# Optimization experiments

Measured on AMD Instinct MI355X. Metric: run time of the kernel, lower is better.

## Reference

```python
import jax, jax.numpy as jnp
import numpy as np

EMBED_DIM = 1024
PROJ_DIM = 64
B, S = 8, 2048


def setup_inputs() -> dict:
    key = jax.random.key(0)
    k1, k2, k3 = jax.random.split(key, 3)
    context = jax.random.normal(k1, (S, B, EMBED_DIM), dtype=jnp.float32)
    prior = jax.random.uniform(k2, (B, S), dtype=jnp.float32)
    # xavier_uniform for (2*proj_dim, embed_dim)
    bound = float(np.sqrt(6.0 / (2 * PROJ_DIM + EMBED_DIM)))
    proj_weight = jax.random.uniform(k3, (2 * PROJ_DIM, EMBED_DIM), dtype=jnp.float32,
                                     minval=-bound, maxval=bound)
    proj_bias = jnp.zeros((2 * PROJ_DIM,), dtype=jnp.float32)
    return {"context": context, "prior": prior,
            "proj_weight": proj_weight, "proj_bias": proj_bias}


def reference(context, prior, proj_weight, proj_bias):
    # context: (S, B, E) -> (B, S, E)
    x = jnp.transpose(context, (1, 0, 2))
    b, s, e = x.shape
    qk = jnp.einsum('bse,pe->bsp', x, proj_weight) + proj_bias  # (B,S,2P)
    query, key = jnp.split(qk, 2, axis=2)
    # neighbor scores, scaled by embed_dim (as in the original)
    fwd = jnp.sum(query[:, :-1] * key[:, 1:], axis=-1) / e   # (B,S-1) score i<->i+1
    bwd = jnp.sum(query[:, 1:] * key[:, :-1], axis=-1) / e   # (B,S-1) score i<->i-1
    ninf = jnp.full((b, 1), -jnp.inf, dtype=x.dtype)
    score = jnp.stack([jnp.concatenate([fwd, ninf], axis=1),
                       jnp.concatenate([ninf, bwd], axis=1)], axis=-1)  # (B,S,2)
    prob = jax.nn.softmax(score, axis=-1)
    # torch .roll(shifts=-1) with no dims flattens the whole tensor: reproduce that
    shift_prob = jnp.roll(prob[:, :, 1].reshape(-1), -1).reshape(b, s)
    prob0 = jnp.sqrt(prob[:, :, 0] * shift_prob + 1e-6)      # (B,S)
    neighbor_attn = prior + (1.0 - prior) * prob0
    log_prob = jnp.log(neighbor_attn)
    # Original places log_prob[:, :-1] on the superdiagonal and hits it with
    # triu matmuls on both sides: C[i,j] = sum_{m=i}^{j-1} log_prob[m] for j>i.
    # Equivalent O(n^2): prefix sums cs[t] = sum_{m<t} log_prob[m].
    cs = jnp.concatenate([jnp.zeros((b, 1), dtype=x.dtype),
                          jnp.cumsum(log_prob[:, :-1], axis=1)], axis=1)  # (B,S)
    D = cs[:, None, :] - cs[:, :, None]            # D[b,i,j] = cs[j]-cs[i]
    i_idx = jnp.arange(s)
    upper = i_idx[None, :] > i_idx[:, None]        # (S,S) j>i
    M = jnp.where(upper[None], D, -D)              # C + C^T (symmetric)
    constituent_attn = jnp.exp(M)
    diag = i_idx[None, :] == i_idx[:, None]
    constituent_attn = jnp.where(diag[None], jnp.zeros((), x.dtype), constituent_attn)
    return constituent_attn, neighbor_attn
```

## Files before the change

### kernel.cpp

```cpp
#include <hip/hip_runtime.h>
#include <cstdint>
#include <cstddef>

#define E_DIM 1024
#define PD 64
#define NP 128
#define B_DIM 8
#define S_DIM 2048
#define M_TOT (B_DIM * S_DIM)

#define KH 512
#define BM 64
#define BK 32
#define NCH (KH / BK)

typedef __attribute__((ext_vector_type(8))) short short8v;
typedef __attribute__((ext_vector_type(4))) float f32x4;

__device__ __forceinline__ void gload16(const float* g, float* l) {
    __builtin_amdgcn_global_load_lds(
        (const __attribute__((address_space(1))) unsigned int*)g,
        (__attribute__((address_space(3))) unsigned int*)(uintptr_t)l,
        16, 0, 0);
}

__device__ __forceinline__ void cvt_hilo(const f32x4 v0, const f32x4 v1,
                                         short8v& h, short8v& l) {
    const unsigned MSK = 0xFFFF0000u;
    unsigned a0 = __float_as_uint(v0.x), a1 = __float_as_uint(v0.y);
    unsigned a2 = __float_as_uint(v0.z), a3 = __float_as_uint(v0.w);
    unsigned a4 = __float_as_uint(v1.x), a5 = __float_as_uint(v1.y);
    unsigned a6 = __float_as_uint(v1.z), a7 = __float_as_uint(v1.w);
    float l0 = v0.x - __uint_as_float(a0 & MSK);
    float l1 = v0.y - __uint_as_float(a1 & MSK);
    float l2 = v0.z - __uint_as_float(a2 & MSK);
    float l3 = v0.w - __uint_as_float(a3 & MSK);
    float l4 = v1.x - __uint_as_float(a4 & MSK);
    float l5 = v1.y - __uint_as_float(a5 & MSK);
    float l6 = v1.z - __uint_as_float(a6 & MSK);
    float l7 = v1.w - __uint_as_float(a7 & MSK);
    union { unsigned u[4]; short8v s; } H, L;
    H.u[0] = (a1 & MSK) | (a0 >> 16);
    H.u[1] = (a3 & MSK) | (a2 >> 16);
    H.u[2] = (a5 & MSK) | (a4 >> 16);
    H.u[3] = (a7 & MSK) | (a6 >> 16);
    L.u[0] = (__float_as_uint(l1) & MSK) | (__float_as_uint(l0) >> 16);
    L.u[1] = (__float_as_uint(l3) & MSK) | (__float_as_uint(l2) >> 16);
    L.u[2] = (__float_as_uint(l5) & MSK) | (__float_as_uint(l4) >> 16);
    L.u[3] = (__float_as_uint(l7) & MSK) | (__float_as_uint(l6) >> 16);
    h = H.s; l = L.s;
}

__global__ __launch_bounds__(256, 2) void gemm_qk(const float* __restrict__ A,
                                                  const float* __restrict__ W,
                                                  float* __restrict__ qk0,
                                                  float* __restrict__ qk1) {
    __shared__ float As[2][BM][BK];
    __shared__ float Ws[2][NP][BK];
    const int tid = threadIdx.x;
    const int kh  = blockIdx.x & 1;
    const int m0  = (blockIdx.x >> 1) * BM;
    const int k0  = kh * KH;
    const int w   = __builtin_amdgcn_readfirstlane(tid >> 6);
    const int ln  = tid & 63;

    const int lr   = ln >> 3;
    const int gsrc = ((ln & 7) ^ lr) << 2;
    const float* aS = A + (size_t)(m0 + w * 16 + lr) * E_DIM + k0 + gsrc;
    const float* wS = W + (size_t)(w * 32 + lr) * E_DIM + k0 + gsrc;

    const int row16 = ln & 15;
    const int kq    = ln >> 4;
    const int wm    = (w >> 1) * 32;
    const int wn    = (w & 1) * 64;
    const int sg0   = (((kq << 1) | 0) ^ (row16 & 7)) << 2;
    const int sg1   = (((kq << 1) | 1) ^ (row16 & 7)) << 2;

    float* qkP = kh ? qk1 : qk0;

    f32x4 acc[2][4];
#pragma unroll
    for (int i = 0; i < 2; ++i)
#pragma unroll
        for (int j = 0; j < 4; ++j) acc[i][j] = (f32x4){0.f, 0.f, 0.f, 0.f};

#define STAGE(BUF, KOFF)                                                       \
    {                                                                          \
        gload16(aS + (KOFF),               &As[BUF][w * 16][0]);               \
        gload16(aS + (KOFF) + 8 * E_DIM,   &As[BUF][w * 16 + 8][0]);           \
        gload16(wS + (KOFF),               &Ws[BUF][w * 32][0]);               \
        gload16(wS + (KOFF) + 8 * E_DIM,   &Ws[BUF][w * 32 + 8][0]);           \
        gload16(wS + (KOFF) + 16 * E_DIM,  &Ws[BUF][w * 32 + 16][0]);          \
        gload16(wS + (KOFF) + 24 * E_DIM,  &Ws[BUF][w * 32 + 24][0]);          \
    }

    STAGE(0, 0)

    for (int ch = 0; ch < NCH; ++ch) {
        const int buf = ch & 1;
        __syncthreads();
        if (ch + 1 < NCH) {
            STAGE(buf ^ 1, (ch + 1) * BK)
        }
        short8v ah[2], al[2], wh[4], wl[4];
#pragma unroll
        for (int fi = 0; fi < 2; ++fi) {
            const float* base = &As[buf][wm + fi * 16 + row16][0];
            const f32x4 v0 = *(const f32x4*)(base + sg0);
            const f32x4 v1 = *(const f32x4*)(base + sg1);
            cvt_hilo(v0, v1, ah[fi], al[fi]);
        }
#pragma unroll
        for (int fj = 0; fj < 4; ++fj) {
            const float* base = &Ws[buf][wn + fj * 16 + row16][0];
            const f32x4 v0 = *(const f32x4*)(base + sg0);
            const f32x4 v1 = *(const f32x4*)(base + sg1);
            cvt_hilo(v0, v1, wh[fj], wl[fj]);
        }
#pragma unroll
        for (int fi = 0; fi < 2; ++fi)
#pragma unroll
            for (int fj = 0; fj < 4; ++fj) {
                acc[fi][fj] = __builtin_amdgcn_mfma_f32_16x16x32_bf16(
                    ah[fi], wh[fj], acc[fi][fj], 0, 0, 0);
                acc[fi][fj] = __builtin_amdgcn_mfma_f32_16x16x32_bf16(
                    ah[fi], wl[fj], acc[fi][fj], 0, 0, 0);
                acc[fi][fj] = __builtin_amdgcn_mfma_f32_16x16x32_bf16(
                    al[fi], wh[fj], acc[fi][fj], 0, 0, 0);
            }
    }
#undef STAGE

#pragma unroll
    for (int fi = 0; fi < 2; ++fi)
#pragma unroll
        for (int fj = 0; fj < 4; ++fj) {
#pragma unroll
            for (int r = 0; r < 4; ++r) {
                const int m = m0 + wm + fi * 16 + kq * 4 + r;
                const int p = wn + fj * 16 + row16;
                qkP[(size_t)m * NP + p] = acc[fi][fj][r];
            }
        }
}

__global__ __launch_bounds__(256) void neighbor_probs(const float* __restrict__ qk0,
                                                      const float* __restrict__ qk1,
                                                      const float* __restrict__ bias,
                                                      float* __restrict__ p0,
                                                      float* __restrict__ p1) {
    const int m = blockIdx.x * 4 + (threadIdx.x >> 6);
    const int lane = threadIdx.x & 63;
    const int s = m >> 3;
    const int b = m & 7;

    const float bq = bias[lane];
    const float bk = bias[PD + lane];
    const size_t oq = (size_t)m * NP + lane;
    const float q = qk0[oq] + qk1[oq] + bq;
    float kn = 0.f, kp = 0.f;
    if (s < S_DIM - 1) {
        const size_t o = (size_t)(m + B_DIM) * NP + PD + lane;
        kn = qk0[o] + qk1[o] + bk;
    }
    if (s > 0) {
        const size_t o = (size_t)(m - B_DIM) * NP + PD + lane;
        kp = qk0[o] + qk1[o] + bk;
    }
    float f = q * kn;
    float g = q * kp;
#pragma unroll
    for (int off = 32; off; off >>= 1) {
        f += __shfl_xor(f, off);
        g += __shfl_xor(g, off);
    }
    if (lane == 0) {
        const float s0 = f * (1.f / (float)E_DIM);
        const float s1 = g * (1.f / (float)E_DIM);
        float P0, P1;
        if (s == S_DIM - 1) { P0 = 0.f; P1 = 1.f; }
        else if (s == 0)    { P0 = 1.f; P1 = 0.f; }
        else {
            const float mx = fmaxf(s0, s1);
            const float e0 = __expf(s0 - mx), e1 = __expf(s1 - mx);
            const float inv = 1.f / (e0 + e1);
            P0 = e0 * inv; P1 = e1 * inv;
        }
        p0[b * S_DIM + s] = P0;
        p1[b * S_DIM + s] = P1;
    }
}

__global__ __launch_bounds__(256) void combine_scan(const float* __restrict__ p0,
                                                    const float* __restrict__ p1,
                                                    const float* __restrict__ prior,
                                                    float* __restrict__ out_na,
                                                    float* __restrict__ cs) {
    const int b = blockIdx.x;
    const int tid = threadIdx.x;
    __shared__ float sh[256];

    const int base = b * S_DIM + tid * 8;
    float incl[8];
    float run = 0.f;
#pragma unroll
    for (int u = 0; u < 8; ++u) {
        const int fidx = base + u;
        int nf = fidx + 1;
        if (nf == B_DIM * S_DIM) nf = 0;
        const float P0 = p0[fidx];
        const float sp = p1[nf];
        const float pr = prior[fidx];
        const float na = pr + (1.f - pr) * sqrtf(P0 * sp + 1e-6f);
        out_na[fidx] = na;
        run += __logf(na);
        incl[u] = run;
    }
    sh[tid] = run;
    __syncthreads();
    for (int off = 1; off < 256; off <<= 1) {
        float v = sh[tid];
        if (tid >= off) v += sh[tid - off];
        __syncthreads();
        sh[tid] = v;
        __syncthreads();
    }
    const float offset = (tid > 0) ? sh[tid - 1] : 0.f;
#pragma unroll
    for (int u = 0; u < 8; ++u) {
        cs[base + u] = offset + ((u > 0) ? incl[u - 1] : 0.f);
    }
}

__global__ __launch_bounds__(256) void big_out(const float* __restrict__ cs,
                                               float* __restrict__ out) {
    const int bi = blockIdx.x;
    const int b = bi >> 11;
    const int i = bi & (S_DIM - 1);
    const float ci = cs[b * S_DIM + i];
    const float* crow = cs + (size_t)b * S_DIM;
    float* orow = out + (size_t)bi * S_DIM;
    const int j0 = threadIdx.x * 8;
#pragma unroll
    for (int h = 0; h < 2; ++h) {
        const int j = j0 + h * 4;
        const float4 cj = *(const float4*)&crow[j];
        float4 o;
        {
            const int jj = j + 0; const float m = (jj > i) ? (cj.x - ci) : (ci - cj.x);
            o.x = (jj == i) ? 0.f : __expf(m);
        }
        {
            const int jj = j + 1; const float m = (jj > i) ? (cj.y - ci) : (ci - cj.y);
            o.y = (jj == i) ? 0.f : __expf(m);
        }
        {
            const int jj = j + 2; const float m = (jj > i) ? (cj.z - ci) : (ci - cj.z);
            o.z = (jj == i) ? 0.f : __expf(m);
        }
        {
            const int jj = j + 3; const float m = (jj > i) ? (cj.w - ci) : (ci - cj.w);
            o.w = (jj == i) ? 0.f : __expf(m);
        }
        *(float4*)&orow[j] = o;
    }
}

extern "C" void kernel_launch(void* const* d_in, const int* in_sizes, int n_in,
                              void* d_out, int out_size, void* d_ws, size_t ws_size,
                              hipStream_t stream) {
    const float* context = (const float*)d_in[0];
    const float* prior   = (const float*)d_in[1];
    const float* W       = (const float*)d_in[2];
    const float* bias    = (const float*)d_in[3];
    float* out = (float*)d_out;

    float* qk0 = (float*)d_ws;
    float* p0  = qk0 + (size_t)M_TOT * NP;
    float* p1  = p0 + M_TOT;
    float* cs  = p1 + M_TOT;
    float* qk1 = out;
    float* na_out = out + (size_t)B_DIM * S_DIM * S_DIM;

    gemm_qk<<<(M_TOT / BM) * 2, 256, 0, stream>>>(context, W, qk0, qk1);
    neighbor_probs<<<M_TOT / 4, 256, 0, stream>>>(qk0, qk1, bias, p0, p1);
    combine_scan<<<B_DIM, 256, 0, stream>>>(p0, p1, prior, na_out, cs);
    big_out<<<M_TOT, 256, 0, stream>>>(cs, out);
}
```

Measured before the change: 66.62 us.

## Pre-split weights into bf16 hi/lo images and drop split-K in QK GEMM

A new kernel converts the projection weight once per call into packed bf16 hi/lo images laid out for direct LDS staging. The GEMM then skips per-tile weight conversion, runs over the full K without split-K, and uses smaller 32-row tiles with each wave owning 32 output columns. Bias is added in the GEMM epilogue, so the neighbor kernel reads one qk buffer instead of summing two partials. The big output kernel also switches to nontemporal stores. The cost is an extra launch and loss of the split-K parallelism, with a longer K loop per block.

New measurement: 84.66 us. 27.1% more time.

```diff
diff --git a/kernel.cpp b/kernel.cpp
--- a/kernel.cpp
+++ b/kernel.cpp
@@ -9,15 +9,14 @@
 #define S_DIM 2048
 #define M_TOT (B_DIM * S_DIM)
 
-#define KH 512
-#define BM 64
+#define BMR 32
 #define BK 32
-#define NCH (KH / BK)
+#define NCH (E_DIM / BK)
 
 typedef __attribute__((ext_vector_type(8))) short short8v;
 typedef __attribute__((ext_vector_type(4))) float f32x4;
 
-__device__ __forceinline__ void gload16(const float* g, float* l) {
+__device__ __forceinline__ void gload16(const void* g, void* l) {
     __builtin_amdgcn_global_load_lds(
         (const __attribute__((address_space(1))) unsigned int*)g,
         (__attribute__((address_space(3))) unsigned int*)(uintptr_t)l,
@@ -51,47 +50,64 @@
     h = H.s; l = L.s;
 }
 
+__global__ __launch_bounds__(256) void conv_w(const float* __restrict__ W,
+                                              ushort* __restrict__ hiImg,
+                                              ushort* __restrict__ loImg) {
+    const int t = blockIdx.x * 256 + threadIdx.x;
+    const int c  = t & 127;
+    const int q  = (t >> 7) & 3;
+    const int ch = t >> 9;
+    const float* src = W + (size_t)c * E_DIM + ch * 32 + q * 8;
+    const f32x4 v0 = *(const f32x4*)src;
+    const f32x4 v1 = *(const f32x4*)(src + 4);
+    short8v h, l;
+    cvt_hilo(v0, v1, h, l);
+    const size_t off = ((size_t)(ch * 4 + q) * NP + c) * 8;
+    *(short8v*)&hiImg[off] = h;
+    *(short8v*)&loImg[off] = l;
+}
+
 __global__ __launch_bounds__(256, 2) void gemm_qk(const float* __restrict__ A,
-                                                  const float* __restrict__ W,
-                                                  float* __restrict__ qk0,
-                                                  float* __restrict__ qk1) {
-    __shared__ float As[2][BM][BK];
-    __shared__ float Ws[2][NP][BK];
+                                                  const ushort* __restrict__ hiImg,
+                                                  const ushort* __restrict__ loImg,
+                                                  const float* __restrict__ bias,
+                                                  float* __restrict__ qk) {
+    __shared__ __align__(16) float  As[2][BMR][BK];
+    __shared__ __align__(16) ushort Whi[2][4][NP][8];
+    __shared__ __align__(16) ushort Wlo[2][4][NP][8];
     const int tid = threadIdx.x;
-    const int kh  = blockIdx.x & 1;
-    const int m0  = (blockIdx.x >> 1) * BM;
-    const int k0  = kh * KH;
+    const int m0  = blockIdx.x * BMR;
     const int w   = __builtin_amdgcn_readfirstlane(tid >> 6);
     const int ln  = tid & 63;
-
-    const int lr   = ln >> 3;
-    const int gsrc = ((ln & 7) ^ lr) << 2;
-    const float* aS = A + (size_t)(m0 + w * 16 + lr) * E_DIM + k0 + gsrc;
-    const float* wS = W + (size_t)(w * 32 + lr) * E_DIM + k0 + gsrc;
-
+    const int lr  = ln >> 3;
+    const int g8  = ln & 7;
     const int row16 = ln & 15;
     const int kq    = ln >> 4;
-    const int wm    = (w >> 1) * 32;
-    const int wn    = (w & 1) * 64;
-    const int sg0   = (((kq << 1) | 0) ^ (row16 & 7)) << 2;
-    const int sg1   = (((kq << 1) | 1) ^ (row16 & 7)) << 2;
-
-    float* qkP = kh ? qk1 : qk0;
-
-    f32x4 acc[2][4];
+    const int r7    = row16 & 7;
+    const int sg0 = ((((kq << 1) | 0) ^ r7) & 7) << 2;
+    const int sg1 = ((((kq << 1) | 1) ^ r7) & 7) << 2;
+
+    const float*  aS = A + (size_t)(m0 + w * 8 + lr) * E_DIM + ((g8 ^ lr) << 2);
+    const ushort* hS = hiImg + (size_t)(w * 2) * 512 + ln * 8;
+    const ushort* lS = loImg + (size_t)(w * 2) * 512 + ln * 8;
+
+    float bias2[2];
+    bias2[0] = bias[w * 32 + row16];
+    bias2[1] = bias[w * 32 + 16 + row16];
+
+    f32x4 acc[2][2];
 #pragma unroll
     for (int i = 0; i < 2; ++i)
 #pragma unroll
-        for (int j = 0; j < 4; ++j) acc[i][j] = (f32x4){0.f, 0.f, 0.f, 0.f};
-
-#define STAGE(BUF, KOFF)                                                       \
-    {                                                                          \
-        gload16(aS + (KOFF),               &As[BUF][w * 16][0]);               \
-        gload16(aS + (KOFF) + 8 * E_DIM,   &As[BUF][w * 16 + 8][0]);           \
-        gload16(wS + (KOFF),               &Ws[BUF][w * 32][0]);               \
-        gload16(wS + (KOFF) + 8 * E_DIM,   &Ws[BUF][w * 32 + 8][0]);           \
-        gload16(wS + (KOFF) + 16 * E_DIM,  &Ws[BUF][w * 32 + 16][0]);          \
-        gload16(wS + (KOFF) + 24 * E_DIM,  &Ws[BUF][w * 32 + 24][0]);          \
+        for (int j = 0; j < 2; ++j) acc[i][j] = (f32x4){0.f, 0.f, 0.f, 0.f};
+
+#define STAGE(BUF, CH)                                                          \
+    {                                                                           \
+        gload16(aS + (size_t)(CH) * BK, &As[BUF][w * 8][0]);                    \
+        gload16(hS + (size_t)(CH) * 4096,       (ushort*)Whi[BUF] + (w * 2) * 512);       \
+        gload16(hS + (size_t)(CH) * 4096 + 512, (ushort*)Whi[BUF] + (w * 2 + 1) * 512);   \
+        gload16(lS + (size_t)(CH) * 4096,       (ushort*)Wlo[BUF] + (w * 2) * 512);       \
+        gload16(lS + (size_t)(CH) * 4096 + 512, (ushort*)Wlo[BUF] + (w * 2 + 1) * 512);   \
     }
 
     STAGE(0, 0)
@@ -100,27 +116,26 @@
         const int buf = ch & 1;
         __syncthreads();
         if (ch + 1 < NCH) {
-            STAGE(buf ^ 1, (ch + 1) * BK)
-        }
-        short8v ah[2], al[2], wh[4], wl[4];
+            STAGE(buf ^ 1, ch + 1)
+        }
+        short8v ah[2], al[2];
 #pragma unroll
         for (int fi = 0; fi < 2; ++fi) {
-            const float* base = &As[buf][wm + fi * 16 + row16][0];
+            const float* base = &As[buf][fi * 16 + row16][0];
             const f32x4 v0 = *(const f32x4*)(base + sg0);
             const f32x4 v1 = *(const f32x4*)(base + sg1);
             cvt_hilo(v0, v1, ah[fi], al[fi]);
         }
-#pragma unroll
-        for (int fj = 0; fj < 4; ++fj) {
-            const float* base = &Ws[buf][wn + fj * 16 + row16][0];
-            const f32x4 v0 = *(const f32x4*)(base + sg0);
-            const f32x4 v1 = *(const f32x4*)(base + sg1);
-            cvt_hilo(v0, v1, wh[fj], wl[fj]);
+        short8v wh[2], wl[2];
+#pragma unroll
+        for (int fj = 0; fj < 2; ++fj) {
+            wh[fj] = *(const short8v*)&Whi[buf][kq][w * 32 + fj * 16 + row16][0];
+            wl[fj] = *(const short8v*)&Wlo[buf][kq][w * 32 + fj * 16 + row16][0];
         }
 #pragma unroll
         for (int fi = 0; fi < 2; ++fi)
 #pragma unroll
-            for (int fj = 0; fj < 4; ++fj) {
+            for (int fj = 0; fj < 2; ++fj) {
                 acc[fi][fj] = __builtin_amdgcn_mfma_f32_16x16x32_bf16(
                     ah[fi], wh[fj], acc[fi][fj], 0, 0, 0);
                 acc[fi][fj] = __builtin_amdgcn_mfma_f32_16x16x32_bf16(
@@ -134,19 +149,17 @@
 #pragma unroll
     for (int fi = 0; fi < 2; ++fi)
 #pragma unroll
-        for (int fj = 0; fj < 4; ++fj) {
+        for (int fj = 0; fj < 2; ++fj) {
 #pragma unroll
             for (int r = 0; r < 4; ++r) {
-                const int m = m0 + wm + fi * 16 + kq * 4 + r;
-                const int p = wn + fj * 16 + row16;
-                qkP[(size_t)m * NP + p] = acc[fi][fj][r];
+                const int m = m0 + fi * 16 + kq * 4 + r;
+                const int p = w * 32 + fj * 16 + row16;
+                qk[(size_t)m * NP + p] = acc[fi][fj][r] + bias2[fj];
             }
         }
 }
 
-__global__ __launch_bounds__(256) void neighbor_probs(const float* __restrict__ qk0,
-                                                      const float* __restrict__ qk1,
-                                                      const float* __restrict__ bias,
+__global__ __launch_bounds__(256) void neighbor_probs(const float* __restrict__ qk,
                                                       float* __restrict__ p0,
                                                       float* __restrict__ p1) {
     const int m = blockIdx.x * 4 + (threadIdx.x >> 6);
@@ -154,19 +167,9 @@
     const int s = m >> 3;
     const int b = m & 7;
 
-    const float bq = bias[lane];
-    const float bk = bias[PD + lane];
-    const size_t oq = (size_t)m * NP + lane;
-    const float q = qk0[oq] + qk1[oq] + bq;
-    float kn = 0.f, kp = 0.f;
-    if (s < S_DIM - 1) {
-        const size_t o = (size_t)(m + B_DIM) * NP + PD + lane;
-        kn = qk0[o] + qk1[o] + bk;
-    }
-    if (s > 0) {
-        const size_t o = (size_t)(m - B_DIM) * NP + PD + lane;
-        kp = qk0[o] + qk1[o] + bk;
-    }
+    const float q = qk[(size_t)m * NP + lane];
+    const float kn = (s < S_DIM - 1) ? qk[(size_t)(m + B_DIM) * NP + PD + lane] : 0.f;
+    const float kp = (s > 0) ? qk[(size_t)(m - B_DIM) * NP + PD + lane] : 0.f;
     float f = q * kn;
     float g = q * kp;
 #pragma unroll
@@ -244,8 +247,8 @@
 #pragma unroll
     for (int h = 0; h < 2; ++h) {
         const int j = j0 + h * 4;
-        const float4 cj = *(const float4*)&crow[j];
-        float4 o;
+        const f32x4 cj = *(const f32x4*)&crow[j];
+        f32x4 o;
         {
             const int jj = j + 0; const float m = (jj > i) ? (cj.x - ci) : (ci - cj.x);
             o.x = (jj == i) ? 0.f : __expf(m);
@@ -262,7 +265,7 @@
             const int jj = j + 3; const float m = (jj > i) ? (cj.w - ci) : (ci - cj.w);
             o.w = (jj == i) ? 0.f : __expf(m);
         }
-        *(float4*)&orow[j] = o;
+        __builtin_nontemporal_store(o, (f32x4*)&orow[j]);
     }
 }
 
@@ -275,15 +278,17 @@
     const float* bias    = (const float*)d_in[3];
     float* out = (float*)d_out;
 
-    float* qk0 = (float*)d_ws;
-    float* p0  = qk0 + (size_t)M_TOT * NP;
-    float* p1  = p0 + M_TOT;
-    float* cs  = p1 + M_TOT;
-    float* qk1 = out;
+    float* qk = (float*)d_ws;
+    float* p0 = qk + (size_t)M_TOT * NP;
+    float* p1 = p0 + M_TOT;
+    float* cs = p1 + M_TOT;
+    ushort* hiImg = (ushort*)out;
+    ushort* loImg = hiImg + (size_t)NP * E_DIM;
     float* na_out = out + (size_t)B_DIM * S_DIM * S_DIM;
 
-    gemm_qk<<<(M_TOT / BM) * 2, 256, 0, stream>>>(context, W, qk0, qk1);
-    neighbor_probs<<<M_TOT / 4, 256, 0, stream>>>(qk0, qk1, bias, p0, p1);
+    conv_w<<<64, 256, 0, stream>>>(W, hiImg, loImg);
+    gemm_qk<<<M_TOT / BMR, 256, 0, stream>>>(context, hiImg, loImg, bias, qk);
+    neighbor_probs<<<M_TOT / 4, 256, 0, stream>>>(qk, p0, p1);
     combine_scan<<<B_DIM, 256, 0, stream>>>(p0, p1, prior, na_out, cs);
     big_out<<<M_TOT, 256, 0, stream>>>(cs, out);
 }
```
